# Optimization experiments

Measured on AMD Instinct MI355X. Metric: run time of the kernel, lower is better.

Reference implementation:

```python
import jax, jax.numpy as jnp
import numpy as np

B, N_BINS, D, G = 2048, 200, 128, 100  # batch, bins (MTL_token_num), feature dim, genes per bin


def setup_inputs() -> dict:
    key = jax.random.key(0)
    k_x, k_w = jax.random.split(key)
    MTL_tokens = jax.random.normal(k_x, (B, N_BINS, D), dtype=jnp.float32)
    # Xavier-uniform init per head: bound = sqrt(6 / (fan_in + fan_out))
    bound = float(np.sqrt(6.0 / (D + G)))
    W = jax.random.uniform(k_w, (N_BINS, G, D), dtype=jnp.float32, minval=-bound, maxval=bound)
    b = jnp.zeros((N_BINS, G), dtype=jnp.float32)
    return {"MTL_tokens": MTL_tokens, "W": W, "b": b}


def reference(MTL_tokens, W, b):
    # Original: for each bin idx, head_idx(MTL_tokens[:, idx]) -> [B, G], collected as a list
    # of length N_BINS, then every scalar is unpacked in (bin, batch, gene) order.
    # Batched grouped GEMM over bins: [B,N,D] x [N,G,D] -> [N,B,G]
    y = jnp.einsum('bnd,ngd->nbg', MTL_tokens, W) + b[:, None, :]
    # activation is None in this config; flatten in (bin, batch, gene) order == the
    # scalar-unpacking double loop of the original module.
    return y.reshape(-1)
```

## Files before the change

### kernel.cpp

```cpp
#include <hip/hip_runtime.h>
#include <hip/hip_bf16.h>

#define NB    200
#define BSZ   2048
#define DD    128
#define GG    100
#define WROWS 112
#define ROWB  256
#define WIMG  (WROWS * ROWB)
#define NTILE (NB * 16)
#define NBLK  512

typedef __attribute__((ext_vector_type(8))) short  short8;
typedef __attribute__((ext_vector_type(4))) float  f32x4;
typedef __attribute__((ext_vector_type(4))) int    i32x4;

__device__ __forceinline__ unsigned f2bf_pack(float lo, float hi) {
    unsigned ulo = __builtin_bit_cast(unsigned, lo);
    ulo += 0x7FFFu + ((ulo >> 16) & 1u);
    unsigned uhi = __builtin_bit_cast(unsigned, hi);
    uhi += 0x7FFFu + ((uhi >> 16) & 1u);
    return (ulo >> 16) | (uhi & 0xFFFF0000u);
}

__device__ __forceinline__ void gload_lds16(const void* g, void* l) {
    __builtin_amdgcn_global_load_lds(
        (const __attribute__((address_space(1))) unsigned int*)g,
        (__attribute__((address_space(3))) unsigned int*)l, 16, 0, 0);
}

#define WAIT_LGKM0() do { asm volatile("" ::: "memory");     \
                          __builtin_amdgcn_s_waitcnt(0xC07F);\
                          __builtin_amdgcn_sched_barrier(0); \
                          __builtin_amdgcn_wave_barrier();   \
                          asm volatile("" ::: "memory"); } while (0)

#define BARRIER_LGKM() do { asm volatile("" ::: "memory");      \
                            __builtin_amdgcn_s_waitcnt(0xC07F); \
                            __builtin_amdgcn_s_barrier();       \
                            __builtin_amdgcn_sched_barrier(0);  \
                            asm volatile("" ::: "memory"); } while (0)

#define BARRIER_VM0() do { asm volatile("s_waitcnt vmcnt(0) lgkmcnt(0)" ::: "memory"); \
                           __builtin_amdgcn_s_barrier();        \
                           __builtin_amdgcn_sched_barrier(0);   \
                           asm volatile("" ::: "memory"); } while (0)

__global__ __launch_bounds__(256) void wconv_kernel(
    const float* __restrict__ W, unsigned char* __restrict__ ws)
{
    const int gidx = blockIdx.x * 256 + threadIdx.x;
    if (gidx >= NB * WROWS * 16) return;
    const int gr  = gidx & 15;
    const int row = (gidx >> 4) % WROWS;
    const int n   = gidx / (WROWS * 16);
    i32x4 pack = (i32x4){0, 0, 0, 0};
    if (row < GG) {
        const float* src = W + ((size_t)n * GG + row) * DD + gr * 8;
        const f32x4 a = *reinterpret_cast<const f32x4*>(src);
        const f32x4 b = *reinterpret_cast<const f32x4*>(src + 4);
        pack.x = (int)f2bf_pack(a[0], a[1]);
        pack.y = (int)f2bf_pack(a[2], a[3]);
        pack.z = (int)f2bf_pack(b[0], b[1]);
        pack.w = (int)f2bf_pack(b[2], b[3]);
    }
    const int off = row * ROWB + ((gr * 16) ^ ((row & 7) << 4));
    *reinterpret_cast<i32x4*>(ws + (size_t)n * WIMG + off) = pack;
}

__device__ __forceinline__ void stage_tile(char* buf, const unsigned char* WS,
                                           int n, int lane, int wid) {
    const unsigned char* src = WS + (size_t)n * WIMG;
    #pragma unroll
    for (int i = 0; i < 7; ++i) {
        const int c = i * 4 + wid;
        gload_lds16(src + c * 1024 + lane * 16, buf + c * 1024);
    }
}

__device__ __forceinline__ void load_x(f32x4 (&raw)[2][4][2], const float* X,
                                       int tile, int wid, int l15, int lhi) {
    const int n = tile >> 4;
    const int rowbase = (tile & 15) * 128 + wid * 32;
    #pragma unroll
    for (int rf = 0; rf < 2; ++rf) {
        const float* xrow = X + ((size_t)(rowbase + rf * 16 + l15) * NB + n) * DD + lhi * 8;
        #pragma unroll
        for (int ks = 0; ks < 4; ++ks) {
            raw[rf][ks][0] = *reinterpret_cast<const f32x4*>(xrow + ks * 32);
            raw[rf][ks][1] = *reinterpret_cast<const f32x4*>(xrow + ks * 32 + 4);
        }
    }
}

__device__ __forceinline__ void conv_x(const f32x4 (&raw)[2][4][2],
                                       short8 (&areg)[2][4]) {
    #pragma unroll
    for (int rf = 0; rf < 2; ++rf)
        #pragma unroll
        for (int ks = 0; ks < 4; ++ks) {
            const f32x4 a = raw[rf][ks][0];
            const f32x4 b = raw[rf][ks][1];
            i32x4 pk;
            pk.x = (int)f2bf_pack(a[0], a[1]);
            pk.y = (int)f2bf_pack(a[2], a[3]);
            pk.z = (int)f2bf_pack(b[0], b[1]);
            pk.w = (int)f2bf_pack(b[2], b[3]);
            areg[rf][ks] = __builtin_bit_cast(short8, pk);
        }
}

__device__ __forceinline__ bool tile_body(int tile,
    const float* __restrict__ X, const float* __restrict__ Bias,
    float* __restrict__ Out, const unsigned char* __restrict__ WS,
    char* bufC, char* bufN,
    short8 (&aregC)[2][4], short8 (&aregN)[2][4], f32x4 (&raw)[2][4][2],
    int lane, int wid, int l15, int lhi)
{
    const int n       = tile >> 4;
    const int rowbase = (tile & 15) * 128 + wid * 32;
    const int tn      = tile + NBLK;
    const bool hasnext = (tn < NTILE);

    if (hasnext) {
        stage_tile(bufN, WS, tn >> 4, lane, wid);
        load_x(raw, X, tn, wid, l15, lhi);
    }
    float bias[7];
    #pragma unroll
    for (int cf = 0; cf < 7; ++cf) {
        const int g = cf * 16 + l15;
        bias[cf] = (g < GG) ? Bias[n * GG + g] : 0.0f;
    }

    f32x4 acc[2][7];
    #pragma unroll
    for (int rf = 0; rf < 2; ++rf)
        #pragma unroll
        for (int cf = 0; cf < 7; ++cf)
            acc[rf][cf] = (f32x4){0.f, 0.f, 0.f, 0.f};

    #pragma unroll
    for (int cf = 0; cf < 7; ++cf) {
        const int g    = cf * 16 + l15;
        const int rowb = g * ROWB;
        const int swz  = (g & 7) << 4;
        #pragma unroll
        for (int ks = 0; ks < 4; ++ks) {
            const int off = rowb + (((lhi * 16) + ks * 64) ^ swz);
            const i32x4 braw = *reinterpret_cast<const i32x4*>(bufC + off);
            const short8 bfrag = __builtin_bit_cast(short8, braw);
            acc[0][cf] = __builtin_amdgcn_mfma_f32_16x16x32_bf16(aregC[0][ks], bfrag, acc[0][cf], 0, 0, 0);
            acc[1][cf] = __builtin_amdgcn_mfma_f32_16x16x32_bf16(aregC[1][ks], bfrag, acc[1][cf], 0, 0, 0);
        }
    }

    BARRIER_LGKM();

    float* lds_f = reinterpret_cast<float*>(bufC + wid * 6400);
    #pragma unroll
    for (int rf = 0; rf < 2; ++rf) {
        #pragma unroll
        for (int cf = 0; cf < 7; ++cf) {
            const int g = cf * 16 + l15;
            if (g < GG) {
                #pragma unroll
                for (int j = 0; j < 4; ++j)
                    lds_f[(lhi * 4 + j) * GG + g] = acc[rf][cf][j] + bias[cf];
            }
        }
        WAIT_LGKM0();
        const char* rgn = bufC + wid * 6400;
        char* dst = (char*)(Out + ((size_t)n * BSZ + rowbase + rf * 16) * GG);
        #pragma unroll
        for (int it = 0; it < 7; ++it) {
            const int c = it * 64 + lane;
            if (c < 400) {
                const i32x4 v = *reinterpret_cast<const i32x4*>(rgn + c * 16);
                __builtin_nontemporal_store(v, reinterpret_cast<i32x4*>(dst + c * 16));
            }
        }
        WAIT_LGKM0();
    }

    if (hasnext) conv_x(raw, aregN);

    BARRIER_VM0();
    return hasnext;
}

__global__ __launch_bounds__(256, 2) void mtl_heads_pipe(
    const float* __restrict__ X, const float* __restrict__ Bias,
    const unsigned char* __restrict__ WS, float* __restrict__ Out)
{
    const int tid  = threadIdx.x;
    const int lane = tid & 63;
    const int wid  = tid >> 6;
    const int l15  = lane & 15;
    const int lhi  = lane >> 4;

    __shared__ __align__(16) char smem[2 * WIMG];
    char* bufA = smem;
    char* bufB = smem + WIMG;

    short8 aregA[2][4], aregB[2][4];
    f32x4  raw[2][4][2];

    int t = blockIdx.x;
    stage_tile(bufA, WS, t >> 4, lane, wid);
    load_x(raw, X, t, wid, l15, lhi);
    BARRIER_VM0();
    conv_x(raw, aregA);

    for (;;) {
        if (!tile_body(t, X, Bias, Out, WS, bufA, bufB, aregA, aregB, raw,
                       lane, wid, l15, lhi)) break;
        t += NBLK;
        if (!tile_body(t, X, Bias, Out, WS, bufB, bufA, aregB, aregA, raw,
                       lane, wid, l15, lhi)) break;
        t += NBLK;
    }
}

__global__ __launch_bounds__(256, 4) void mtl_heads_fallback(
    const float* __restrict__ X, const float* __restrict__ W,
    const float* __restrict__ Bias, float* __restrict__ Out)
{
    const int n     = blockIdx.y;
    const int mtile = blockIdx.x;
    const int tid   = threadIdx.x;
    const int lane  = tid & 63;
    const int wid   = tid >> 6;
    const int l15   = lane & 15;
    const int lhi   = lane >> 4;

    __shared__ __align__(16) char smem[WIMG];

    {
        const int rsub = tid >> 4;
        const int k0   = (tid & 15) * 8;
        #pragma unroll
        for (int it = 0; it < 7; ++it) {
            const int row = it * 16 + rsub;
            i32x4 pack = (i32x4){0, 0, 0, 0};
            if (row < GG) {
                const float* s = W + ((size_t)n * GG + row) * DD + k0;
                const f32x4 a = *reinterpret_cast<const f32x4*>(s);
                const f32x4 b = *reinterpret_cast<const f32x4*>(s + 4);
                pack.x = (int)f2bf_pack(a[0], a[1]);
                pack.y = (int)f2bf_pack(a[2], a[3]);
                pack.z = (int)f2bf_pack(b[0], b[1]);
                pack.w = (int)f2bf_pack(b[2], b[3]);
            }
            const int off = row * ROWB + ((k0 * 2) ^ ((row & 7) << 4));
            *reinterpret_cast<i32x4*>(smem + off) = pack;
        }
    }

    const int rowbase = mtile * 128 + wid * 32;
    f32x4 raw[2][4][2];
    load_x(raw, X, n * 16 + mtile, wid, l15, lhi);
    float bias[7];
    #pragma unroll
    for (int cf = 0; cf < 7; ++cf) {
        const int g = cf * 16 + l15;
        bias[cf] = (g < GG) ? Bias[n * GG + g] : 0.0f;
    }
    short8 areg[2][4];
    conv_x(raw, areg);

    __syncthreads();

    f32x4 acc[2][7];
    #pragma unroll
    for (int rf = 0; rf < 2; ++rf)
        #pragma unroll
        for (int cf = 0; cf < 7; ++cf)
            acc[rf][cf] = (f32x4){0.f, 0.f, 0.f, 0.f};

    #pragma unroll
    for (int cf = 0; cf < 7; ++cf) {
        const int g    = cf * 16 + l15;
        const int rowb = g * ROWB;
        const int swz  = (g & 7) << 4;
        #pragma unroll
        for (int ks = 0; ks < 4; ++ks) {
            const int off = rowb + (((lhi * 16) + ks * 64) ^ swz);
            const i32x4 braw = *reinterpret_cast<const i32x4*>(smem + off);
            const short8 bfrag = __builtin_bit_cast(short8, braw);
            acc[0][cf] = __builtin_amdgcn_mfma_f32_16x16x32_bf16(areg[0][ks], bfrag, acc[0][cf], 0, 0, 0);
            acc[1][cf] = __builtin_amdgcn_mfma_f32_16x16x32_bf16(areg[1][ks], bfrag, acc[1][cf], 0, 0, 0);
        }
    }

    __syncthreads();

    float* lds_f = reinterpret_cast<float*>(smem + wid * 6400);
    #pragma unroll
    for (int rf = 0; rf < 2; ++rf) {
        #pragma unroll
        for (int cf = 0; cf < 7; ++cf) {
            const int g = cf * 16 + l15;
            if (g < GG) {
                #pragma unroll
                for (int j = 0; j < 4; ++j)
                    lds_f[(lhi * 4 + j) * GG + g] = acc[rf][cf][j] + bias[cf];
            }
        }
        WAIT_LGKM0();
        const char* rgn = smem + wid * 6400;
        char* dst = (char*)(Out + ((size_t)n * BSZ + rowbase + rf * 16) * GG);
        #pragma unroll
        for (int it = 0; it < 7; ++it) {
            const int c = it * 64 + lane;
            if (c < 400) {
                const i32x4 v = *reinterpret_cast<const i32x4*>(rgn + c * 16);
                *reinterpret_cast<i32x4*>(dst + c * 16) = v;
            }
        }
        WAIT_LGKM0();
    }
}

extern "C" void kernel_launch(void* const* d_in, const int* in_sizes, int n_in,
                              void* d_out, int out_size, void* d_ws, size_t ws_size,
                              hipStream_t stream) {
    (void)in_sizes; (void)n_in; (void)out_size;
    const float* X    = (const float*)d_in[0];
    const float* W    = (const float*)d_in[1];
    const float* Bias = (const float*)d_in[2];
    float* Out        = (float*)d_out;
    const size_t wsneed = (size_t)NB * WIMG;
    if (ws_size >= wsneed) {
        wconv_kernel<<<(NB * WROWS * 16 + 255) / 256, 256, 0, stream>>>(W, (unsigned char*)d_ws);
        mtl_heads_pipe<<<dim3(NBLK), 256, 0, stream>>>(X, Bias, (const unsigned char*)d_ws, Out);
    } else {
        mtl_heads_fallback<<<dim3(16, NB), 256, 0, stream>>>(X, W, Bias, Out);
    }
}
```

Before: 74.86 us.

## Replace persistent double-buffered pipeline with per-bin blocks reusing staged weights

The persistent kernel, which double-buffered weight tiles across 512 blocks, is replaced by 800 blocks. Each block stages one bin's bf16 weight image (100 rows) into LDS once and reuses it across 4 consecutive 128-row M tiles, prefetching the next X tile into registers while the current one computes. LDS use drops from two full weight images to one plus per-wave scratch, allowing 3 blocks per CU, and block-wide barriers inside the loop go away. In exchange, the next bin's weights are no longer overlapped across tiles and each block re-stages weights at its start.

```diff
diff --git a/kernel.cpp b/kernel.cpp
--- a/kernel.cpp
+++ b/kernel.cpp
@@ -8,8 +8,9 @@
 #define WROWS 112
 #define ROWB  256
 #define WIMG  (WROWS * ROWB)
-#define NTILE (NB * 16)
-#define NBLK  512
+#define WLDS  (100 * ROWB)
+#define SCR   6400
+#define NBLK2 800
 
 typedef __attribute__((ext_vector_type(8))) short  short8;
 typedef __attribute__((ext_vector_type(4))) float  f32x4;
@@ -34,17 +35,6 @@
                           __builtin_amdgcn_sched_barrier(0); \
                           __builtin_amdgcn_wave_barrier();   \
                           asm volatile("" ::: "memory"); } while (0)
-
-#define BARRIER_LGKM() do { asm volatile("" ::: "memory");      \
-                            __builtin_amdgcn_s_waitcnt(0xC07F); \
-                            __builtin_amdgcn_s_barrier();       \
-                            __builtin_amdgcn_sched_barrier(0);  \
-                            asm volatile("" ::: "memory"); } while (0)
-
-#define BARRIER_VM0() do { asm volatile("s_waitcnt vmcnt(0) lgkmcnt(0)" ::: "memory"); \
-                           __builtin_amdgcn_s_barrier();        \
-                           __builtin_amdgcn_sched_barrier(0);   \
-                           asm volatile("" ::: "memory"); } while (0)
 
 __global__ __launch_bounds__(256) void wconv_kernel(
     const float* __restrict__ W, unsigned char* __restrict__ ws)
@@ -68,20 +58,21 @@
     *reinterpret_cast<i32x4*>(ws + (size_t)n * WIMG + off) = pack;
 }
 
-__device__ __forceinline__ void stage_tile(char* buf, const unsigned char* WS,
+__device__ __forceinline__ void stage_w100(char* buf, const unsigned char* WS,
                                            int n, int lane, int wid) {
     const unsigned char* src = WS + (size_t)n * WIMG;
     #pragma unroll
-    for (int i = 0; i < 7; ++i) {
+    for (int i = 0; i < 6; ++i) {
         const int c = i * 4 + wid;
         gload_lds16(src + c * 1024 + lane * 16, buf + c * 1024);
     }
+    if (wid == 0)
+        gload_lds16(src + 24 * 1024 + lane * 16, buf + 24 * 1024);
 }
 
 __device__ __forceinline__ void load_x(f32x4 (&raw)[2][4][2], const float* X,
-                                       int tile, int wid, int l15, int lhi) {
-    const int n = tile >> 4;
-    const int rowbase = (tile & 15) * 128 + wid * 32;
+                                       int n, int mtile, int wid, int l15, int lhi) {
+    const int rowbase = mtile * 128 + wid * 32;
     #pragma unroll
     for (int rf = 0; rf < 2; ++rf) {
         const float* xrow = X + ((size_t)(rowbase + rf * 16 + l15) * NB + n) * DD + lhi * 8;
@@ -110,86 +101,7 @@
         }
 }
 
-__device__ __forceinline__ bool tile_body(int tile,
-    const float* __restrict__ X, const float* __restrict__ Bias,
-    float* __restrict__ Out, const unsigned char* __restrict__ WS,
-    char* bufC, char* bufN,
-    short8 (&aregC)[2][4], short8 (&aregN)[2][4], f32x4 (&raw)[2][4][2],
-    int lane, int wid, int l15, int lhi)
-{
-    const int n       = tile >> 4;
-    const int rowbase = (tile & 15) * 128 + wid * 32;
-    const int tn      = tile + NBLK;
-    const bool hasnext = (tn < NTILE);
-
-    if (hasnext) {
-        stage_tile(bufN, WS, tn >> 4, lane, wid);
-        load_x(raw, X, tn, wid, l15, lhi);
-    }
-    float bias[7];
-    #pragma unroll
-    for (int cf = 0; cf < 7; ++cf) {
-        const int g = cf * 16 + l15;
-        bias[cf] = (g < GG) ? Bias[n * GG + g] : 0.0f;
-    }
-
-    f32x4 acc[2][7];
-    #pragma unroll
-    for (int rf = 0; rf < 2; ++rf)
-        #pragma unroll
-        for (int cf = 0; cf < 7; ++cf)
-            acc[rf][cf] = (f32x4){0.f, 0.f, 0.f, 0.f};
-
-    #pragma unroll
-    for (int cf = 0; cf < 7; ++cf) {
-        const int g    = cf * 16 + l15;
-        const int rowb = g * ROWB;
-        const int swz  = (g & 7) << 4;
-        #pragma unroll
-        for (int ks = 0; ks < 4; ++ks) {
-            const int off = rowb + (((lhi * 16) + ks * 64) ^ swz);
-            const i32x4 braw = *reinterpret_cast<const i32x4*>(bufC + off);
-            const short8 bfrag = __builtin_bit_cast(short8, braw);
-            acc[0][cf] = __builtin_amdgcn_mfma_f32_16x16x32_bf16(aregC[0][ks], bfrag, acc[0][cf], 0, 0, 0);
-            acc[1][cf] = __builtin_amdgcn_mfma_f32_16x16x32_bf16(aregC[1][ks], bfrag, acc[1][cf], 0, 0, 0);
-        }
-    }
-
-    BARRIER_LGKM();
-
-    float* lds_f = reinterpret_cast<float*>(bufC + wid * 6400);
-    #pragma unroll
-    for (int rf = 0; rf < 2; ++rf) {
-        #pragma unroll
-        for (int cf = 0; cf < 7; ++cf) {
-            const int g = cf * 16 + l15;
-            if (g < GG) {
-                #pragma unroll
-                for (int j = 0; j < 4; ++j)
-                    lds_f[(lhi * 4 + j) * GG + g] = acc[rf][cf][j] + bias[cf];
-            }
-        }
-        WAIT_LGKM0();
-        const char* rgn = bufC + wid * 6400;
-        char* dst = (char*)(Out + ((size_t)n * BSZ + rowbase + rf * 16) * GG);
-        #pragma unroll
-        for (int it = 0; it < 7; ++it) {
-            const int c = it * 64 + lane;
-            if (c < 400) {
-                const i32x4 v = *reinterpret_cast<const i32x4*>(rgn + c * 16);
-                __builtin_nontemporal_store(v, reinterpret_cast<i32x4*>(dst + c * 16));
-            }
-        }
-        WAIT_LGKM0();
-    }
-
-    if (hasnext) conv_x(raw, aregN);
-
-    BARRIER_VM0();
-    return hasnext;
-}
-
-__global__ __launch_bounds__(256, 2) void mtl_heads_pipe(
+__global__ __launch_bounds__(256, 3) void mtl_heads_bin(
     const float* __restrict__ X, const float* __restrict__ Bias,
     const unsigned char* __restrict__ WS, float* __restrict__ Out)
 {
@@ -199,26 +111,80 @@
     const int l15  = lane & 15;
     const int lhi  = lane >> 4;
 
-    __shared__ __align__(16) char smem[2 * WIMG];
-    char* bufA = smem;
-    char* bufB = smem + WIMG;
-
-    short8 aregA[2][4], aregB[2][4];
-    f32x4  raw[2][4][2];
-
-    int t = blockIdx.x;
-    stage_tile(bufA, WS, t >> 4, lane, wid);
-    load_x(raw, X, t, wid, l15, lhi);
-    BARRIER_VM0();
-    conv_x(raw, aregA);
-
-    for (;;) {
-        if (!tile_body(t, X, Bias, Out, WS, bufA, bufB, aregA, aregB, raw,
-                       lane, wid, l15, lhi)) break;
-        t += NBLK;
-        if (!tile_body(t, X, Bias, Out, WS, bufB, bufA, aregB, aregA, raw,
-                       lane, wid, l15, lhi)) break;
-        t += NBLK;
+    const int n   = blockIdx.x >> 2;
+    const int mt0 = (blockIdx.x & 3) * 4;
+
+    __shared__ __align__(16) char smem[WLDS + 4 * SCR];
+
+    stage_w100(smem, WS, n, lane, wid);
+    f32x4 raw[2][4][2];
+    load_x(raw, X, n, mt0, wid, l15, lhi);
+    float bias[7];
+    #pragma unroll
+    for (int cf = 0; cf < 7; ++cf) {
+        const int g = cf * 16 + l15;
+        bias[cf] = (g < GG) ? Bias[n * GG + g] : 0.0f;
+    }
+    short8 areg[2][4];
+    conv_x(raw, areg);
+    __syncthreads();
+
+    char* scratch = smem + WLDS + wid * SCR;
+
+    for (int mt = 0; mt < 4; ++mt) {
+        const int mtile = mt0 + mt;
+        if (mt < 3) load_x(raw, X, n, mtile + 1, wid, l15, lhi);
+
+        f32x4 acc[2][7];
+        #pragma unroll
+        for (int rf = 0; rf < 2; ++rf)
+            #pragma unroll
+            for (int cf = 0; cf < 7; ++cf)
+                acc[rf][cf] = (f32x4){0.f, 0.f, 0.f, 0.f};
+
+        #pragma unroll
+        for (int cf = 0; cf < 7; ++cf) {
+            const int g = cf * 16 + l15;
+            const int r = (g < GG) ? g : 99;
+            const int rowb = r * ROWB;
+            const int swz  = (r & 7) << 4;
+            #pragma unroll
+            for (int ks = 0; ks < 4; ++ks) {
+                const int off = rowb + (((lhi * 16) + ks * 64) ^ swz);
+                const i32x4 braw = *reinterpret_cast<const i32x4*>(smem + off);
+                const short8 bfrag = __builtin_bit_cast(short8, braw);
+                acc[0][cf] = __builtin_amdgcn_mfma_f32_16x16x32_bf16(areg[0][ks], bfrag, acc[0][cf], 0, 0, 0);
+                acc[1][cf] = __builtin_amdgcn_mfma_f32_16x16x32_bf16(areg[1][ks], bfrag, acc[1][cf], 0, 0, 0);
+            }
+        }
+
+        const int rowbase = mtile * 128 + wid * 32;
+        float* lds_f = reinterpret_cast<float*>(scratch);
+        #pragma unroll
+        for (int rf = 0; rf < 2; ++rf) {
+            #pragma unroll
+            for (int cf = 0; cf < 7; ++cf) {
+                const int g = cf * 16 + l15;
+                if (g < GG) {
+                    #pragma unroll
+                    for (int j = 0; j < 4; ++j)
+                        lds_f[(lhi * 4 + j) * GG + g] = acc[rf][cf][j] + bias[cf];
+                }
+            }
+            WAIT_LGKM0();
+            char* dst = (char*)(Out + ((size_t)n * BSZ + rowbase + rf * 16) * GG);
+            #pragma unroll
+            for (int it = 0; it < 7; ++it) {
+                const int c = it * 64 + lane;
+                if (c < 400) {
+                    const i32x4 v = *reinterpret_cast<const i32x4*>(scratch + c * 16);
+                    __builtin_nontemporal_store(v, reinterpret_cast<i32x4*>(dst + c * 16));
+                }
+            }
+            WAIT_LGKM0();
+        }
+
+        if (mt < 3) conv_x(raw, areg);
     }
 }
 
@@ -259,7 +225,7 @@
 
     const int rowbase = mtile * 128 + wid * 32;
     f32x4 raw[2][4][2];
-    load_x(raw, X, n * 16 + mtile, wid, l15, lhi);
+    load_x(raw, X, n, mtile, wid, l15, lhi);
     float bias[7];
     #pragma unroll
     for (int cf = 0; cf < 7; ++cf) {
@@ -295,7 +261,7 @@
 
     __syncthreads();
 
-    float* lds_f = reinterpret_cast<float*>(smem + wid * 6400);
+    float* lds_f = reinterpret_cast<float*>(smem + wid * SCR);
     #pragma unroll
     for (int rf = 0; rf < 2; ++rf) {
         #pragma unroll
@@ -308,7 +274,7 @@
             }
         }
         WAIT_LGKM0();
-        const char* rgn = smem + wid * 6400;
+        const char* rgn = smem + wid * SCR;
         char* dst = (char*)(Out + ((size_t)n * BSZ + rowbase + rf * 16) * GG);
         #pragma unroll
         for (int it = 0; it < 7; ++it) {
@@ -333,7 +299,7 @@
     const size_t wsneed = (size_t)NB * WIMG;
     if (ws_size >= wsneed) {
         wconv_kernel<<<(NB * WROWS * 16 + 255) / 256, 256, 0, stream>>>(W, (unsigned char*)d_ws);
-        mtl_heads_pipe<<<dim3(NBLK), 256, 0, stream>>>(X, Bias, (const unsigned char*)d_ws, Out);
+        mtl_heads_bin<<<dim3(NBLK2), 256, 0, stream>>>(X, Bias, (const unsigned char*)d_ws, Out);
     } else {
         mtl_heads_fallback<<<dim3(16, NB), 256, 0, stream>>>(X, W, Bias, Out);
     }
```

Result: slower. 96.16 us (+28.4%).
